# Performance work log

Hardware: AMD Instinct MI355X
Metric: run time of the kernel (lower is better)

## Reference

```python
import jax, jax.numpy as jnp
import numpy as np

ALPHA = 0.1


def setup_inputs() -> dict:
    key = jax.random.key(0)
    k1, k2, k3, k4 = jax.random.split(key, 4)
    B, S, D = 64, 2048, 512
    n_mask, n_unmask = 1536, 512
    return {
        "outputs": jax.random.normal(k1, (B, S, D), dtype=jnp.float32),
        "orig_image": jax.random.normal(k2, (B, S, D), dtype=jnp.float32),
        "mask_id": jax.random.randint(k3, (B, n_mask), 0, S, dtype=jnp.int64),
        "unmask_id": jax.random.randint(k4, (B, n_unmask), 0, S, dtype=jnp.int64),
    }


def _per_sample_mse(outputs, orig, idx):
    # gather [B, n_idx, D] rows, then MSE (mean reduction) per sample -> [B]
    pred = jnp.take_along_axis(outputs, idx[:, :, None], axis=1)
    tgt = jnp.take_along_axis(orig, idx[:, :, None], axis=1)
    return jnp.mean((pred - tgt) ** 2, axis=(1, 2))


def reference(outputs, orig_image, mask_id, unmask_id):
    # sum_i loss_i / b  ==  mean over batch of per-sample MSE
    masked = _per_sample_mse(outputs, orig_image, mask_id)    # [B]
    unmasked = _per_sample_mse(outputs, orig_image, unmask_id)  # [B]
    return jnp.mean(masked) + ALPHA * jnp.mean(unmasked)
```

## Files before the change

kernel.cpp:

```cpp
#include <hip/hip_runtime.h>

constexpr int B_DIM   = 64;
constexpr int S_DIM   = 2048;
constexpr int D_DIM   = 512;
constexpr int NMASK   = 1536;
constexpr int NUNMASK = 512;
constexpr float ALPHA = 0.1f;

constexpr int N_MASK_TOT = B_DIM * NMASK;
constexpr int N_UN_TOT   = B_DIM * NUNMASK;
constexpr int N_IDX_TOT  = N_MASK_TOT + N_UN_TOT;
constexpr int ROWS_TOTAL = B_DIM * S_DIM;

__global__ __launch_bounds__(256) void build_weights(
    const int* __restrict__ mask_id,
    const int* __restrict__ unmask_id,
    float*     __restrict__ w)
{
    const float wm = 1.0f / (float)((long long)B_DIM * NMASK   * D_DIM);
    const float wu = ALPHA / (float)((long long)B_DIM * NUNMASK * D_DIM);

    const int i = blockIdx.x * blockDim.x + threadIdx.x;
    if (i >= N_IDX_TOT) return;
    if (i < N_MASK_TOT) {
        const int b   = i / NMASK;
        const int idx = mask_id[i];
        atomicAdd(&w[(b << 11) + idx], wm);
    } else {
        const int j   = i - N_MASK_TOT;
        const int b   = j >> 9;
        const int idx = unmask_id[j];
        atomicAdd(&w[(b << 11) + idx], wu);
    }
}

constexpr int BLOCK2          = 256;
constexpr int ROWS_PER_BLOCK  = 64;
constexpr int GRID2           = ROWS_TOTAL / ROWS_PER_BLOCK;

__global__ __launch_bounds__(BLOCK2) void weighted_sse(
    const float* __restrict__ outputs,
    const float* __restrict__ orig,
    const float* __restrict__ w,
    float*       __restrict__ out)
{
    __shared__ float wsh[ROWS_PER_BLOCK];
    __shared__ float sdata[BLOCK2 / 64];

    const int base = blockIdx.x * ROWS_PER_BLOCK;
    if (threadIdx.x < ROWS_PER_BLOCK)
        wsh[threadIdx.x] = w[base + threadIdx.x];
    __syncthreads();

    const int wid  = threadIdx.x >> 6;
    const int lane = threadIdx.x & 63;

    float acc = 0.0f;

    #pragma unroll
    for (int i = 0; i < ROWS_PER_BLOCK / 4; ++i) {
        const int   rlocal = i * 4 + wid;
        const float wgt    = wsh[rlocal];
        if (wgt != 0.0f) {
            const size_t off = (size_t)(base + rlocal) * D_DIM;
            const float4* po = (const float4*)(outputs + off);
            const float4* pt = (const float4*)(orig    + off);
            const float4 o0 = po[lane];
            const float4 o1 = po[lane + 64];
            const float4 t0 = pt[lane];
            const float4 t1 = pt[lane + 64];
            float s = 0.0f;
            {
                const float dx = o0.x - t0.x, dy = o0.y - t0.y;
                const float dz = o0.z - t0.z, dw = o0.w - t0.w;
                s += dx * dx + dy * dy + dz * dz + dw * dw;
            }
            {
                const float dx = o1.x - t1.x, dy = o1.y - t1.y;
                const float dz = o1.z - t1.z, dw = o1.w - t1.w;
                s += dx * dx + dy * dy + dz * dz + dw * dw;
            }
            acc = fmaf(wgt, s, acc);
        }
    }

    #pragma unroll
    for (int off = 32; off > 0; off >>= 1)
        acc += __shfl_down(acc, off, 64);

    if (lane == 0) sdata[wid] = acc;
    __syncthreads();

    if (threadIdx.x == 0) {
        atomicAdd(out, sdata[0] + sdata[1] + sdata[2] + sdata[3]);
    }
}

__global__ __launch_bounds__(256) void mae_loss_kernel(
    const float* __restrict__ outputs,
    const float* __restrict__ orig,
    const int*   __restrict__ mask_id,
    const int*   __restrict__ unmask_id,
    float*       __restrict__ out)
{
    const int lane_in_row  = threadIdx.x & 127;
    const int row_in_block = threadIdx.x >> 7;

    const float wm = 1.0f / (float)((long long)B_DIM * NMASK   * D_DIM);
    const float wu = ALPHA / (float)((long long)B_DIM * NUNMASK * D_DIM);

    float acc = 0.0f;
    for (int r = blockIdx.x * 2 + row_in_block; r < ROWS_TOTAL; r += 2048 * 2) {
        const int b = r >> 11;
        const int j = r & 2047;
        int   idx;
        float w;
        if (j < NMASK) { idx = mask_id[b * NMASK + j]; w = wm; }
        else           { idx = unmask_id[b * NUNMASK + (j - NMASK)]; w = wu; }
        const size_t row_off = ((size_t)b * S_DIM + (size_t)idx) * D_DIM;
        const float4* po = (const float4*)(outputs + row_off);
        const float4* pt = (const float4*)(orig    + row_off);
        const float4 o = po[lane_in_row];
        const float4 t = pt[lane_in_row];
        const float dx = o.x - t.x, dy = o.y - t.y;
        const float dz = o.z - t.z, dw = o.w - t.w;
        acc += w * (dx * dx + dy * dy + dz * dz + dw * dw);
    }
    #pragma unroll
    for (int off = 32; off > 0; off >>= 1)
        acc += __shfl_down(acc, off, 64);
    __shared__ float sdata[4];
    const int wid = threadIdx.x >> 6;
    if ((threadIdx.x & 63) == 0) sdata[wid] = acc;
    __syncthreads();
    if (threadIdx.x == 0) {
        float s = 0.0f;
        #pragma unroll
        for (int i = 0; i < 4; ++i) s += sdata[i];
        atomicAdd(out, s);
    }
}

extern "C" void kernel_launch(void* const* d_in, const int* in_sizes, int n_in,
                              void* d_out, int out_size, void* d_ws, size_t ws_size,
                              hipStream_t stream) {
    const float* outputs   = (const float*)d_in[0];
    const float* orig      = (const float*)d_in[1];
    const int*   mask_id   = (const int*)d_in[2];
    const int*   unmask_id = (const int*)d_in[3];
    float* out = (float*)d_out;

    hipMemsetAsync(out, 0, sizeof(float), stream);

    const size_t wbytes = (size_t)ROWS_TOTAL * sizeof(float);
    if (ws_size >= wbytes) {
        float* w = (float*)d_ws;
        hipMemsetAsync(w, 0, wbytes, stream);
        const int threads = 256;
        const int blocks  = (N_IDX_TOT + threads - 1) / threads;
        build_weights<<<blocks, threads, 0, stream>>>(mask_id, unmask_id, w);
        weighted_sse<<<GRID2, BLOCK2, 0, stream>>>(outputs, orig, w, out);
    } else {
        mae_loss_kernel<<<2048, 256, 0, stream>>>(outputs, orig, mask_id, unmask_id, out);
    }
}
```

Before: 489.2 us.

## Fuse weight building into SSE kernel using per-block shared-memory histograms

Replaces the two-kernel scheme (global atomic weight histogram plus weighted SSE) with one kernel. Each block scans its sample's mask and unmask indices and builds weights for its 64-row window with shared-memory atomics. This removes the workspace memset, the global atomics and a kernel launch, at the cost of every block redundantly reading its sample's index list.

New measurement: 482.4 us. No clear change (-1.4%).

```diff
diff --git a/kernel.cpp b/kernel.cpp
--- a/kernel.cpp
+++ b/kernel.cpp
@@ -7,73 +7,73 @@
 constexpr int NUNMASK = 512;
 constexpr float ALPHA = 0.1f;
 
-constexpr int N_MASK_TOT = B_DIM * NMASK;
-constexpr int N_UN_TOT   = B_DIM * NUNMASK;
-constexpr int N_IDX_TOT  = N_MASK_TOT + N_UN_TOT;
 constexpr int ROWS_TOTAL = B_DIM * S_DIM;
+constexpr int RPB        = 64;
+constexpr int BLOCK      = 256;
+constexpr int GRID       = ROWS_TOTAL / RPB;
+constexpr int BLOCKS_PER_SAMPLE = S_DIM / RPB;
 
-__global__ __launch_bounds__(256) void build_weights(
-    const int* __restrict__ mask_id,
-    const int* __restrict__ unmask_id,
-    float*     __restrict__ w)
+__global__ __launch_bounds__(BLOCK) void fused_mae_loss(
+    const float* __restrict__ outputs,
+    const float* __restrict__ orig,
+    const int*   __restrict__ mask_id,
+    const int*   __restrict__ unmask_id,
+    float*       __restrict__ out)
 {
+    __shared__ float wsh[RPB];
+    __shared__ float sred[BLOCK / 64];
+
+    const int tid = threadIdx.x;
+    const int b   = blockIdx.x >> 5;
+    const int win = (blockIdx.x & (BLOCKS_PER_SAMPLE - 1)) * RPB;
+
+    if (tid < RPB) wsh[tid] = 0.0f;
+    __syncthreads();
+
     const float wm = 1.0f / (float)((long long)B_DIM * NMASK   * D_DIM);
     const float wu = ALPHA / (float)((long long)B_DIM * NUNMASK * D_DIM);
 
-    const int i = blockIdx.x * blockDim.x + threadIdx.x;
-    if (i >= N_IDX_TOT) return;
-    if (i < N_MASK_TOT) {
-        const int b   = i / NMASK;
-        const int idx = mask_id[i];
-        atomicAdd(&w[(b << 11) + idx], wm);
-    } else {
-        const int j   = i - N_MASK_TOT;
-        const int b   = j >> 9;
-        const int idx = unmask_id[j];
-        atomicAdd(&w[(b << 11) + idx], wu);
+    {
+        const int* mp = mask_id + b * NMASK;
+        #pragma unroll
+        for (int k = 0; k < NMASK / BLOCK; ++k) {
+            const int idx = mp[k * BLOCK + tid];
+            const unsigned loc = (unsigned)(idx - win);
+            if (loc < (unsigned)RPB) atomicAdd(&wsh[loc], wm);
+        }
+        const int* up = unmask_id + b * NUNMASK;
+        #pragma unroll
+        for (int k = 0; k < NUNMASK / BLOCK; ++k) {
+            const int idx = up[k * BLOCK + tid];
+            const unsigned loc = (unsigned)(idx - win);
+            if (loc < (unsigned)RPB) atomicAdd(&wsh[loc], wu);
+        }
     }
-}
-
-constexpr int BLOCK2          = 256;
-constexpr int ROWS_PER_BLOCK  = 64;
-constexpr int GRID2           = ROWS_TOTAL / ROWS_PER_BLOCK;
-
-__global__ __launch_bounds__(BLOCK2) void weighted_sse(
-    const float* __restrict__ outputs,
-    const float* __restrict__ orig,
-    const float* __restrict__ w,
-    float*       __restrict__ out)
-{
-    __shared__ float wsh[ROWS_PER_BLOCK];
-    __shared__ float sdata[BLOCK2 / 64];
-
-    const int base = blockIdx.x * ROWS_PER_BLOCK;
-    if (threadIdx.x < ROWS_PER_BLOCK)
-        wsh[threadIdx.x] = w[base + threadIdx.x];
     __syncthreads();
 
-    const int wid  = threadIdx.x >> 6;
-    const int lane = threadIdx.x & 63;
+    const int wid  = tid >> 6;
+    const int lane = tid & 63;
+    const size_t base_off = ((size_t)b * S_DIM + (size_t)win) * D_DIM;
 
     float acc = 0.0f;
 
     #pragma unroll
-    for (int i = 0; i < ROWS_PER_BLOCK / 4; ++i) {
-        const int   rlocal = i * 4 + wid;
-        const float wgt    = wsh[rlocal];
+    for (int i = 0; i < RPB / 4; ++i) {
+        const int   rloc = i * 4 + wid;
+        const float wgt  = wsh[rloc];
         if (wgt != 0.0f) {
-            const size_t off = (size_t)(base + rlocal) * D_DIM;
+            const size_t off = base_off + (size_t)rloc * D_DIM;
             const float4* po = (const float4*)(outputs + off);
             const float4* pt = (const float4*)(orig    + off);
             const float4 o0 = po[lane];
             const float4 o1 = po[lane + 64];
             const float4 t0 = pt[lane];
             const float4 t1 = pt[lane + 64];
-            float s = 0.0f;
+            float s;
             {
                 const float dx = o0.x - t0.x, dy = o0.y - t0.y;
                 const float dz = o0.z - t0.z, dw = o0.w - t0.w;
-                s += dx * dx + dy * dy + dz * dz + dw * dw;
+                s = dx * dx + dy * dy + dz * dz + dw * dw;
             }
             {
                 const float dx = o1.x - t1.x, dy = o1.y - t1.y;
@@ -88,57 +88,11 @@
     for (int off = 32; off > 0; off >>= 1)
         acc += __shfl_down(acc, off, 64);
 
-    if (lane == 0) sdata[wid] = acc;
+    if (lane == 0) sred[wid] = acc;
     __syncthreads();
 
-    if (threadIdx.x == 0) {
-        atomicAdd(out, sdata[0] + sdata[1] + sdata[2] + sdata[3]);
-    }
-}
-
-__global__ __launch_bounds__(256) void mae_loss_kernel(
-    const float* __restrict__ outputs,
-    const float* __restrict__ orig,
-    const int*   __restrict__ mask_id,
-    const int*   __restrict__ unmask_id,
-    float*       __restrict__ out)
-{
-    const int lane_in_row  = threadIdx.x & 127;
-    const int row_in_block = threadIdx.x >> 7;
-
-    const float wm = 1.0f / (float)((long long)B_DIM * NMASK   * D_DIM);
-    const float wu = ALPHA / (float)((long long)B_DIM * NUNMASK * D_DIM);
-
-    float acc = 0.0f;
-    for (int r = blockIdx.x * 2 + row_in_block; r < ROWS_TOTAL; r += 2048 * 2) {
-        const int b = r >> 11;
-        const int j = r & 2047;
-        int   idx;
-        float w;
-        if (j < NMASK) { idx = mask_id[b * NMASK + j]; w = wm; }
-        else           { idx = unmask_id[b * NUNMASK + (j - NMASK)]; w = wu; }
-        const size_t row_off = ((size_t)b * S_DIM + (size_t)idx) * D_DIM;
-        const float4* po = (const float4*)(outputs + row_off);
-        const float4* pt = (const float4*)(orig    + row_off);
-        const float4 o = po[lane_in_row];
-        const float4 t = pt[lane_in_row];
-        const float dx = o.x - t.x, dy = o.y - t.y;
-        const float dz = o.z - t.z, dw = o.w - t.w;
-        acc += w * (dx * dx + dy * dy + dz * dz + dw * dw);
-    }
-    #pragma unroll
-    for (int off = 32; off > 0; off >>= 1)
-        acc += __shfl_down(acc, off, 64);
-    __shared__ float sdata[4];
-    const int wid = threadIdx.x >> 6;
-    if ((threadIdx.x & 63) == 0) sdata[wid] = acc;
-    __syncthreads();
-    if (threadIdx.x == 0) {
-        float s = 0.0f;
-        #pragma unroll
-        for (int i = 0; i < 4; ++i) s += sdata[i];
-        atomicAdd(out, s);
-    }
+    if (tid == 0)
+        atomicAdd(out, sred[0] + sred[1] + sred[2] + sred[3]);
 }
 
 extern "C" void kernel_launch(void* const* d_in, const int* in_sizes, int n_in,
@@ -152,15 +106,5 @@
 
     hipMemsetAsync(out, 0, sizeof(float), stream);
 
-    const size_t wbytes = (size_t)ROWS_TOTAL * sizeof(float);
-    if (ws_size >= wbytes) {
-        float* w = (float*)d_ws;
-        hipMemsetAsync(w, 0, wbytes, stream);
-        const int threads = 256;
-        const int blocks  = (N_IDX_TOT + threads - 1) / threads;
-        build_weights<<<blocks, threads, 0, stream>>>(mask_id, unmask_id, w);
-        weighted_sse<<<GRID2, BLOCK2, 0, stream>>>(outputs, orig, w, out);
-    } else {
-        mae_loss_kernel<<<2048, 256, 0, stream>>>(outputs, orig, mask_id, unmask_id, out);
-    }
+    fused_mae_loss<<<GRID, BLOCK, 0, stream>>>(outputs, orig, mask_id, unmask_id, out);
 }
```
